# Kernel optimization log

Measured on AMD Instinct MI355X. Metric: run time of the kernel, lower is better.

## Reference

```python
import jax, jax.numpy as jnp
import numpy as np


def setup_inputs() -> dict:
    key = jax.random.key(0)
    k1, k2 = jax.random.split(key)
    B, N1, N2, D = 16, 2048, 2048, 300
    X = jax.random.normal(k1, (B, N1, D), dtype=jnp.float32)
    Y = jax.random.normal(k2, (B, N2, D), dtype=jnp.float32)
    return {"X": X, "Y": Y}


def reference(X, Y):
    # Bidirectional co-attention, unscaled.
    # M1: (b, n1, n2), M2: (b, n2, n1)
    M1 = jnp.einsum("bnd,bmd->bnm", X, Y)
    M2 = jnp.einsum("bmd,bnd->bmn", Y, X)
    N1 = jax.nn.softmax(M1, axis=2)
    N2 = jax.nn.softmax(M2, axis=2)
    O1 = jnp.einsum("bnm,bmd->bnd", N1, Y)  # (b, n1, d)
    O2 = jnp.einsum("bmn,bnd->bmd", N2, X)  # (b, n2, d)
    A1 = O1 * X
    A2 = O2 * Y
    return jnp.concatenate((A1, A2), axis=1)
```

## Files before the change

### kernel.cpp

```cpp
#include <hip/hip_runtime.h>

typedef _Float16 f16;
typedef __attribute__((ext_vector_type(8))) _Float16 f16x8;
typedef __attribute__((ext_vector_type(4))) _Float16 f16x4;
typedef __attribute__((ext_vector_type(4))) float f32x4;

#define BATCH 16
#define NSEQ  2048
#define DDIM  300
#define DPK   328
#define DPV   304
#define NTP   2056
#define XF_ELEMS (BATCH*NSEQ*DPK)
#define XT_ELEMS (BATCH*DPV*NTP)

__device__ __forceinline__ void gl_lds16(const void* g, void* l) {
  __builtin_amdgcn_global_load_lds((const __attribute__((address_space(1))) unsigned int*)g,
                                   (__attribute__((address_space(3))) unsigned int*)l, 16, 0, 0);
}

__global__ __launch_bounds__(256) void prep_kernel(const float* __restrict__ X,
                                                   const float* __restrict__ Y,
                                                   f16* __restrict__ Xf, f16* __restrict__ Yf,
                                                   f16* __restrict__ XT, f16* __restrict__ YT) {
  __shared__ float tile[32][33];
  int bz   = blockIdx.z;
  int tsel = bz >> 4, b = bz & 15;
  const float* src = tsel ? Y : X;
  f16* dF = tsel ? Yf : Xf;
  f16* dT = tsel ? YT : XT;
  int d0 = blockIdx.y * 32;
  int q0 = blockIdx.x * 32;
  int tid = threadIdx.x;
  int c = tid & 31, rr = tid >> 5;

  #pragma unroll
  for (int i = 0; i < 4; ++i) {
    int qr = rr + i * 8;
    int q = q0 + qr, d = d0 + c;
    float v = 0.f;
    if (q < NSEQ && d < DDIM) v = src[(size_t)b * NSEQ * DDIM + (size_t)q * DDIM + d];
    tile[c][qr] = v;
    if (q < NSEQ && d < DPK) dF[(size_t)b * NSEQ * DPK + (size_t)q * DPK + d] = (f16)v;
  }
  __syncthreads();
  #pragma unroll
  for (int i = 0; i < 4; ++i) {
    int dr = rr + i * 8;
    int d = d0 + dr, q = q0 + c;
    if (d < DPV && q < NTP) dT[(size_t)b * DPV * NTP + (size_t)d * NTP + q] = (f16)tile[dr][c];
  }
}

__global__ __launch_bounds__(512, 1) void attn_kernel(const f16* __restrict__ Xf,
                                                      const f16* __restrict__ Yf,
                                                      const f16* __restrict__ XT,
                                                      const f16* __restrict__ YT,
                                                      float* __restrict__ out) {
  __shared__ __align__(16) f16 Ksh[2][64][DPK];
  __shared__ __align__(16) f16 VTsh[DPV][72];
  __shared__ __align__(16) f16 Psh[4][32][72];
  __shared__ float2 Mx[4][2][16];

  int idx = blockIdx.x;
  int swz = (idx & 7) * 64 + (idx >> 3);
  int qt  = swz & 15;
  int b   = (swz >> 4) & 15;
  int dir = swz >> 8;

  const f16* Qsrc = dir ? Yf : Xf;
  const f16* Ksrc = dir ? Xf : Yf;
  const f16* Vts  = dir ? XT : YT;

  const size_t bq = (size_t)b * NSEQ * DPK;
  const size_t bt = (size_t)b * DPV * NTP;

  int tid = threadIdx.x;
  int lane = tid & 63, wid = tid >> 6;
  int qg = wid >> 1, mem = wid & 1;
  int l15 = lane & 15, g = lane >> 4;
  int qbase = qt * 128 + qg * 32;

  f16x8 qf[2][10];
  #pragma unroll
  for (int qi = 0; qi < 2; ++qi) {
    const f16* qrow = Qsrc + bq + (size_t)(qbase + qi * 16 + l15) * DPK + g * 8;
    #pragma unroll
    for (int ks = 0; ks < 10; ++ks) qf[qi][ks] = *(const f16x8*)(qrow + ks * 32);
  }

  const int dtoff = mem ? 10 : 0;
  const int ndt   = mem ? 9 : 10;

  f32x4 O[10][2];
  #pragma unroll
  for (int dt = 0; dt < 10; ++dt) {
    O[dt][0] = (f32x4){0.f, 0.f, 0.f, 0.f};
    O[dt][1] = (f32x4){0.f, 0.f, 0.f, 0.f};
  }
  float m0 = -3.0e38f, m1 = -3.0e38f;
  float l0 = 0.f, l1 = 0.f;

  const char* gK0 = (const char*)(Ksrc + bq);
  const char* gV0 = (const char*)(Vts + bt);

  auto stageK = [&](int tt, int buf) {
    const char* gK = gK0 + (size_t)tt * (64 * DPK * 2);
    char* lK = (char*)&Ksh[buf][0][0];
    #pragma unroll
    for (int i = 0; i < 6; ++i) {
      int c = i * 512 + tid;
      if (c < 2624) gl_lds16(gK + c * 16, lK + c * 16);
    }
  };
  auto stageV = [&](int tt) {
    const char* gV = gV0 + (size_t)tt * 128;
    char* lV = (char*)&VTsh[0][0];
    #pragma unroll
    for (int i = 0; i < 6; ++i) {
      int c = i * 512 + tid;
      if (c < 2736) {
        int row = (int)((unsigned)c / 9u), slot = c - row * 9;
        gl_lds16(gV + (size_t)row * (NTP * 2) + slot * 16, lV + c * 16);
      }
    }
  };

  stageK(0, 0);
  asm volatile("s_waitcnt vmcnt(0)" ::: "memory");
  __builtin_amdgcn_s_barrier();
  __builtin_amdgcn_sched_barrier(0);

  #pragma unroll 1
  for (int t = 0; t < 32; ++t) {
    int kcur = t & 1;

    f32x4 S[2][2];
    S[0][0] = (f32x4){0.f,0.f,0.f,0.f}; S[0][1] = (f32x4){0.f,0.f,0.f,0.f};
    S[1][0] = (f32x4){0.f,0.f,0.f,0.f}; S[1][1] = (f32x4){0.f,0.f,0.f,0.f};
    __builtin_amdgcn_s_setprio(1);
    if (t > 0) {
      #pragma unroll
      for (int ks = 0; ks < 2; ++ks) {
        f16x8 pb0 = *(const f16x8*)&Psh[qg][l15][ks * 32 + g * 8];
        f16x8 pb1 = *(const f16x8*)&Psh[qg][16 + l15][ks * 32 + g * 8];
        #pragma unroll
        for (int dt = 0; dt < 10; ++dt) {
          if (dt < ndt) {
            f16x8 vf = *(const f16x8*)&VTsh[(dtoff + dt) * 16 + l15][ks * 32 + g * 8];
            O[dt][0] = __builtin_amdgcn_mfma_f32_16x16x32_f16(vf, pb0, O[dt][0], 0, 0, 0);
            O[dt][1] = __builtin_amdgcn_mfma_f32_16x16x32_f16(vf, pb1, O[dt][1], 0, 0, 0);
          }
        }
      }
    }
    #pragma unroll
    for (int ks = 0; ks < 10; ++ks) {
      f16x8 a0 = *(const f16x8*)&Ksh[kcur][mem * 32 + l15][ks * 32 + g * 8];
      f16x8 a1 = *(const f16x8*)&Ksh[kcur][mem * 32 + 16 + l15][ks * 32 + g * 8];
      S[0][0] = __builtin_amdgcn_mfma_f32_16x16x32_f16(a0, qf[0][ks], S[0][0], 0, 0, 0);
      S[0][1] = __builtin_amdgcn_mfma_f32_16x16x32_f16(a0, qf[1][ks], S[0][1], 0, 0, 0);
      S[1][0] = __builtin_amdgcn_mfma_f32_16x16x32_f16(a1, qf[0][ks], S[1][0], 0, 0, 0);
      S[1][1] = __builtin_amdgcn_mfma_f32_16x16x32_f16(a1, qf[1][ks], S[1][1], 0, 0, 0);
    }
    __builtin_amdgcn_s_setprio(0);

    if (t < 31) stageK(t + 1, kcur ^ 1);

    float p0 = fmaxf(fmaxf(fmaxf(S[0][0][0], S[0][0][1]), fmaxf(S[0][0][2], S[0][0][3])),
                     fmaxf(fmaxf(S[1][0][0], S[1][0][1]), fmaxf(S[1][0][2], S[1][0][3])));
    float p1 = fmaxf(fmaxf(fmaxf(S[0][1][0], S[0][1][1]), fmaxf(S[0][1][2], S[0][1][3])),
                     fmaxf(fmaxf(S[1][1][0], S[1][1][1]), fmaxf(S[1][1][2], S[1][1][3])));
    p0 = fmaxf(p0, __shfl_xor(p0, 16, 64)); p0 = fmaxf(p0, __shfl_xor(p0, 32, 64));
    p1 = fmaxf(p1, __shfl_xor(p1, 16, 64)); p1 = fmaxf(p1, __shfl_xor(p1, 32, 64));
    if (g == 0) Mx[qg][mem][l15] = float2{p0, p1};

    asm volatile("s_waitcnt lgkmcnt(0)" ::: "memory");
    __builtin_amdgcn_s_barrier();
    __builtin_amdgcn_sched_barrier(0);

    stageV(t);

    float2 pp = Mx[qg][mem ^ 1][l15];
    float tm0 = fmaxf(p0, pp.x), tm1 = fmaxf(p1, pp.y);

    if (__any(tm0 > m0 + 8.0f)) {
      float mn = fmaxf(m0, tm0), al = __expf(m0 - mn);
      l0 *= al;
      #pragma unroll
      for (int dt = 0; dt < 10; ++dt) {
        O[dt][0][0] *= al; O[dt][0][1] *= al; O[dt][0][2] *= al; O[dt][0][3] *= al;
      }
      m0 = mn;
    }
    if (__any(tm1 > m1 + 8.0f)) {
      float mn = fmaxf(m1, tm1), al = __expf(m1 - mn);
      l1 *= al;
      #pragma unroll
      for (int dt = 0; dt < 10; ++dt) {
        O[dt][1][0] *= al; O[dt][1][1] *= al; O[dt][1][2] *= al; O[dt][1][3] *= al;
      }
      m1 = mn;
    }

    #pragma unroll
    for (int kvt = 0; kvt < 2; ++kvt) {
      f16x4 h0, h1;
      #pragma unroll
      for (int r = 0; r < 4; ++r) {
        float e0 = __expf(S[kvt][0][r] - m0);
        float e1 = __expf(S[kvt][1][r] - m1);
        h0[r] = (f16)e0; h1[r] = (f16)e1;
        l0 += e0; l1 += e1;
      }
      *(f16x4*)&Psh[qg][l15][mem * 32 + kvt * 16 + g * 4]      = h0;
      *(f16x4*)&Psh[qg][16 + l15][mem * 32 + kvt * 16 + g * 4] = h1;
    }

    asm volatile("s_waitcnt lgkmcnt(0) vmcnt(0)" ::: "memory");
    __builtin_amdgcn_s_barrier();
    __builtin_amdgcn_sched_barrier(0);
  }

  {
    __builtin_amdgcn_s_setprio(1);
    #pragma unroll
    for (int ks = 0; ks < 2; ++ks) {
      f16x8 pb0 = *(const f16x8*)&Psh[qg][l15][ks * 32 + g * 8];
      f16x8 pb1 = *(const f16x8*)&Psh[qg][16 + l15][ks * 32 + g * 8];
      #pragma unroll
      for (int dt = 0; dt < 10; ++dt) {
        if (dt < ndt) {
          f16x8 vf = *(const f16x8*)&VTsh[(dtoff + dt) * 16 + l15][ks * 32 + g * 8];
          O[dt][0] = __builtin_amdgcn_mfma_f32_16x16x32_f16(vf, pb0, O[dt][0], 0, 0, 0);
          O[dt][1] = __builtin_amdgcn_mfma_f32_16x16x32_f16(vf, pb1, O[dt][1], 0, 0, 0);
        }
      }
    }
    __builtin_amdgcn_s_setprio(0);
  }

  l0 += __shfl_xor(l0, 16, 64); l0 += __shfl_xor(l0, 32, 64);
  l1 += __shfl_xor(l1, 16, 64); l1 += __shfl_xor(l1, 32, 64);
  if (g == 0) Mx[qg][mem][l15] = float2{l0, l1};
  asm volatile("s_waitcnt lgkmcnt(0)" ::: "memory");
  __builtin_amdgcn_s_barrier();
  __builtin_amdgcn_sched_barrier(0);
  float2 pl = Mx[qg][mem ^ 1][l15];
  float r0 = 1.0f / (l0 + pl.x);
  float r1 = 1.0f / (l1 + pl.y);

  #pragma unroll
  for (int qi = 0; qi < 2; ++qi) {
    float rinv = qi ? r1 : r0;
    int q = qbase + qi * 16 + l15;
    const f16* mrow = Qsrc + bq + (size_t)q * DPK;
    size_t orow = (size_t)b * (4096 * 300) + (size_t)(dir * 2048 + q) * 300;
    #pragma unroll
    for (int dt = 0; dt < 10; ++dt) {
      if (dt < ndt) {
        int d = (dtoff + dt) * 16 + g * 4;
        if (d < 300) {
          f16x4 mu = *(const f16x4*)(mrow + d);
          f32x4 o;
          o[0] = O[dt][qi][0] * rinv * (float)mu[0];
          o[1] = O[dt][qi][1] * rinv * (float)mu[1];
          o[2] = O[dt][qi][2] * rinv * (float)mu[2];
          o[3] = O[dt][qi][3] * rinv * (float)mu[3];
          *(f32x4*)&out[orow + d] = o;
        }
      }
    }
  }
}

extern "C" void kernel_launch(void* const* d_in, const int* in_sizes, int n_in,
                              void* d_out, int out_size, void* d_ws, size_t ws_size,
                              hipStream_t stream) {
  const float* X = (const float*)d_in[0];
  const float* Y = (const float*)d_in[1];
  float* out = (float*)d_out;

  size_t need = (size_t)(2 * XF_ELEMS + 2 * XT_ELEMS) * sizeof(f16);
  if (ws_size < need) return;

  f16* XT = (f16*)d_ws;
  f16* YT = XT + XT_ELEMS;
  f16* Xf = YT + XT_ELEMS;
  f16* Yf = Xf + XF_ELEMS;

  prep_kernel<<<dim3(65, 11, 32), 256, 0, stream>>>(X, Y, Xf, Yf, XT, YT);
  attn_kernel<<<dim3(512), 512, 0, stream>>>(Xf, Yf, XT, YT, out);
}
```

Before: 255.8 us.

## Switch attention MFMAs from 16x16x32 to 32x32x16 tiles with interleaved PV

Replaces the 16x16x32 f16 MFMA tiling with 32x32x16 instructions for both QK^T and PV. Each wave now owns a 32x32 score tile in one accumulator and a 5x32-wide output slice, with the two waves overlapping on d range 144-160. The PV MFMAs are split into two halves interleaved with the QK^T halves to mix the dependency chains. Larger tiles cut LDS fragment loads per FLOP and the number of softmax reductions, at the cost of some redundant PV work in the overlap and different register pressure.

```diff
diff --git a/kernel.cpp b/kernel.cpp
--- a/kernel.cpp
+++ b/kernel.cpp
@@ -4,6 +4,7 @@
 typedef __attribute__((ext_vector_type(8))) _Float16 f16x8;
 typedef __attribute__((ext_vector_type(4))) _Float16 f16x4;
 typedef __attribute__((ext_vector_type(4))) float f32x4;
+typedef __attribute__((ext_vector_type(16))) float f32x16;
 
 #define BATCH 16
 #define NSEQ  2048
@@ -60,7 +61,7 @@
   __shared__ __align__(16) f16 Ksh[2][64][DPK];
   __shared__ __align__(16) f16 VTsh[DPV][72];
   __shared__ __align__(16) f16 Psh[4][32][72];
-  __shared__ float2 Mx[4][2][16];
+  __shared__ float MxS[4][2][32];
 
   int idx = blockIdx.x;
   int swz = (idx & 7) * 64 + (idx >> 3);
@@ -78,28 +79,25 @@
   int tid = threadIdx.x;
   int lane = tid & 63, wid = tid >> 6;
   int qg = wid >> 1, mem = wid & 1;
-  int l15 = lane & 15, g = lane >> 4;
+  int l31 = lane & 31, hi = lane >> 5;
   int qbase = qt * 128 + qg * 32;
 
-  f16x8 qf[2][10];
+  f16x8 qf[20];
+  {
+    const f16* qrow = Qsrc + bq + (size_t)(qbase + l31) * DPK + hi * 8;
+    #pragma unroll
+    for (int ks = 0; ks < 20; ++ks) qf[ks] = *(const f16x8*)(qrow + ks * 16);
+  }
+
+  const int dbase = mem ? 144 : 0;
+  const int dlo   = mem ? 160 : 0;
+
+  f32x16 O[5];
   #pragma unroll
-  for (int qi = 0; qi < 2; ++qi) {
-    const f16* qrow = Qsrc + bq + (size_t)(qbase + qi * 16 + l15) * DPK + g * 8;
-    #pragma unroll
-    for (int ks = 0; ks < 10; ++ks) qf[qi][ks] = *(const f16x8*)(qrow + ks * 32);
-  }
-
-  const int dtoff = mem ? 10 : 0;
-  const int ndt   = mem ? 9 : 10;
-
-  f32x4 O[10][2];
-  #pragma unroll
-  for (int dt = 0; dt < 10; ++dt) {
-    O[dt][0] = (f32x4){0.f, 0.f, 0.f, 0.f};
-    O[dt][1] = (f32x4){0.f, 0.f, 0.f, 0.f};
-  }
-  float m0 = -3.0e38f, m1 = -3.0e38f;
-  float l0 = 0.f, l1 = 0.f;
+  for (int dt = 0; dt < 5; ++dt)
+    #pragma unroll
+    for (int e = 0; e < 16; ++e) O[dt][e] = 0.f;
+  float m = -3.0e38f, l = 0.f;
 
   const char* gK0 = (const char*)(Ksrc + bq);
   const char* gV0 = (const char*)(Vts + bt);
@@ -135,45 +133,53 @@
   for (int t = 0; t < 32; ++t) {
     int kcur = t & 1;
 
-    f32x4 S[2][2];
-    S[0][0] = (f32x4){0.f,0.f,0.f,0.f}; S[0][1] = (f32x4){0.f,0.f,0.f,0.f};
-    S[1][0] = (f32x4){0.f,0.f,0.f,0.f}; S[1][1] = (f32x4){0.f,0.f,0.f,0.f};
+    f32x16 S;
+    #pragma unroll
+    for (int e = 0; e < 16; ++e) S[e] = 0.f;
     __builtin_amdgcn_s_setprio(1);
     if (t > 0) {
       #pragma unroll
       for (int ks = 0; ks < 2; ++ks) {
-        f16x8 pb0 = *(const f16x8*)&Psh[qg][l15][ks * 32 + g * 8];
-        f16x8 pb1 = *(const f16x8*)&Psh[qg][16 + l15][ks * 32 + g * 8];
+        f16x8 pf = *(const f16x8*)&Psh[qg][l31][ks * 16 + hi * 8];
         #pragma unroll
-        for (int dt = 0; dt < 10; ++dt) {
-          if (dt < ndt) {
-            f16x8 vf = *(const f16x8*)&VTsh[(dtoff + dt) * 16 + l15][ks * 32 + g * 8];
-            O[dt][0] = __builtin_amdgcn_mfma_f32_16x16x32_f16(vf, pb0, O[dt][0], 0, 0, 0);
-            O[dt][1] = __builtin_amdgcn_mfma_f32_16x16x32_f16(vf, pb1, O[dt][1], 0, 0, 0);
-          }
+        for (int dt = 0; dt < 5; ++dt) {
+          f16x8 vf = *(const f16x8*)&VTsh[dbase + dt * 32 + l31][ks * 16 + hi * 8];
+          O[dt] = __builtin_amdgcn_mfma_f32_32x32x16_f16(vf, pf, O[dt], 0, 0, 0);
         }
       }
     }
     #pragma unroll
     for (int ks = 0; ks < 10; ++ks) {
-      f16x8 a0 = *(const f16x8*)&Ksh[kcur][mem * 32 + l15][ks * 32 + g * 8];
-      f16x8 a1 = *(const f16x8*)&Ksh[kcur][mem * 32 + 16 + l15][ks * 32 + g * 8];
-      S[0][0] = __builtin_amdgcn_mfma_f32_16x16x32_f16(a0, qf[0][ks], S[0][0], 0, 0, 0);
-      S[0][1] = __builtin_amdgcn_mfma_f32_16x16x32_f16(a0, qf[1][ks], S[0][1], 0, 0, 0);
-      S[1][0] = __builtin_amdgcn_mfma_f32_16x16x32_f16(a1, qf[0][ks], S[1][0], 0, 0, 0);
-      S[1][1] = __builtin_amdgcn_mfma_f32_16x16x32_f16(a1, qf[1][ks], S[1][1], 0, 0, 0);
+      f16x8 a = *(const f16x8*)&Ksh[kcur][mem * 32 + l31][ks * 16 + hi * 8];
+      S = __builtin_amdgcn_mfma_f32_32x32x16_f16(a, qf[ks], S, 0, 0, 0);
+    }
+    if (t > 0) {
+      #pragma unroll
+      for (int ks = 2; ks < 4; ++ks) {
+        f16x8 pf = *(const f16x8*)&Psh[qg][l31][ks * 16 + hi * 8];
+        #pragma unroll
+        for (int dt = 0; dt < 5; ++dt) {
+          f16x8 vf = *(const f16x8*)&VTsh[dbase + dt * 32 + l31][ks * 16 + hi * 8];
+          O[dt] = __builtin_amdgcn_mfma_f32_32x32x16_f16(vf, pf, O[dt], 0, 0, 0);
+        }
+      }
+    }
+    #pragma unroll
+    for (int ks = 10; ks < 20; ++ks) {
+      f16x8 a = *(const f16x8*)&Ksh[kcur][mem * 32 + l31][ks * 16 + hi * 8];
+      S = __builtin_amdgcn_mfma_f32_32x32x16_f16(a, qf[ks], S, 0, 0, 0);
     }
     __builtin_amdgcn_s_setprio(0);
 
     if (t < 31) stageK(t + 1, kcur ^ 1);
 
-    float p0 = fmaxf(fmaxf(fmaxf(S[0][0][0], S[0][0][1]), fmaxf(S[0][0][2], S[0][0][3])),
-                     fmaxf(fmaxf(S[1][0][0], S[1][0][1]), fmaxf(S[1][0][2], S[1][0][3])));
-    float p1 = fmaxf(fmaxf(fmaxf(S[0][1][0], S[0][1][1]), fmaxf(S[0][1][2], S[0][1][3])),
-                     fmaxf(fmaxf(S[1][1][0], S[1][1][1]), fmaxf(S[1][1][2], S[1][1][3])));
-    p0 = fmaxf(p0, __shfl_xor(p0, 16, 64)); p0 = fmaxf(p0, __shfl_xor(p0, 32, 64));
-    p1 = fmaxf(p1, __shfl_xor(p1, 16, 64)); p1 = fmaxf(p1, __shfl_xor(p1, 32, 64));
-    if (g == 0) Mx[qg][mem][l15] = float2{p0, p1};
+    float p = fmaxf(fmaxf(fmaxf(S[0], S[1]), S[2]),
+                    fmaxf(fmaxf(S[3], S[4]), S[5]));
+    p = fmaxf(p, fmaxf(fmaxf(S[6], S[7]), fmaxf(S[8], S[9])));
+    p = fmaxf(p, fmaxf(fmaxf(S[10], S[11]), fmaxf(S[12], S[13])));
+    p = fmaxf(p, fmaxf(S[14], S[15]));
+    p = fmaxf(p, __shfl_xor(p, 32, 64));
+    if (lane < 32) MxS[qg][mem][l31] = p;
 
     asm volatile("s_waitcnt lgkmcnt(0)" ::: "memory");
     __builtin_amdgcn_s_barrier();
@@ -181,40 +187,29 @@
 
     stageV(t);
 
-    float2 pp = Mx[qg][mem ^ 1][l15];
-    float tm0 = fmaxf(p0, pp.x), tm1 = fmaxf(p1, pp.y);
-
-    if (__any(tm0 > m0 + 8.0f)) {
-      float mn = fmaxf(m0, tm0), al = __expf(m0 - mn);
-      l0 *= al;
-      #pragma unroll
-      for (int dt = 0; dt < 10; ++dt) {
-        O[dt][0][0] *= al; O[dt][0][1] *= al; O[dt][0][2] *= al; O[dt][0][3] *= al;
-      }
-      m0 = mn;
-    }
-    if (__any(tm1 > m1 + 8.0f)) {
-      float mn = fmaxf(m1, tm1), al = __expf(m1 - mn);
-      l1 *= al;
-      #pragma unroll
-      for (int dt = 0; dt < 10; ++dt) {
-        O[dt][1][0] *= al; O[dt][1][1] *= al; O[dt][1][2] *= al; O[dt][1][3] *= al;
-      }
-      m1 = mn;
-    }
-
-    #pragma unroll
-    for (int kvt = 0; kvt < 2; ++kvt) {
-      f16x4 h0, h1;
-      #pragma unroll
-      for (int r = 0; r < 4; ++r) {
-        float e0 = __expf(S[kvt][0][r] - m0);
-        float e1 = __expf(S[kvt][1][r] - m1);
-        h0[r] = (f16)e0; h1[r] = (f16)e1;
-        l0 += e0; l1 += e1;
-      }
-      *(f16x4*)&Psh[qg][l15][mem * 32 + kvt * 16 + g * 4]      = h0;
-      *(f16x4*)&Psh[qg][16 + l15][mem * 32 + kvt * 16 + g * 4] = h1;
+    float pp = MxS[qg][mem ^ 1][l31];
+    float tm = fmaxf(p, pp);
+
+    if (__any(tm > m + 8.0f)) {
+      float mn = fmaxf(m, tm), al = __expf(m - mn);
+      l *= al;
+      #pragma unroll
+      for (int dt = 0; dt < 5; ++dt)
+        #pragma unroll
+        for (int e = 0; e < 16; ++e) O[dt][e] *= al;
+      m = mn;
+    }
+
+    #pragma unroll
+    for (int r = 0; r < 4; ++r) {
+      f16x4 h;
+      #pragma unroll
+      for (int j = 0; j < 4; ++j) {
+        float e = __expf(S[4 * r + j] - m);
+        h[j] = (f16)e;
+        l += e;
+      }
+      *(f16x4*)&Psh[qg][l31][mem * 32 + r * 8 + hi * 4] = h;
     }
 
     asm volatile("s_waitcnt lgkmcnt(0) vmcnt(0)" ::: "memory");
@@ -225,49 +220,42 @@
   {
     __builtin_amdgcn_s_setprio(1);
     #pragma unroll
-    for (int ks = 0; ks < 2; ++ks) {
-      f16x8 pb0 = *(const f16x8*)&Psh[qg][l15][ks * 32 + g * 8];
-      f16x8 pb1 = *(const f16x8*)&Psh[qg][16 + l15][ks * 32 + g * 8];
-      #pragma unroll
-      for (int dt = 0; dt < 10; ++dt) {
-        if (dt < ndt) {
-          f16x8 vf = *(const f16x8*)&VTsh[(dtoff + dt) * 16 + l15][ks * 32 + g * 8];
-          O[dt][0] = __builtin_amdgcn_mfma_f32_16x16x32_f16(vf, pb0, O[dt][0], 0, 0, 0);
-          O[dt][1] = __builtin_amdgcn_mfma_f32_16x16x32_f16(vf, pb1, O[dt][1], 0, 0, 0);
-        }
+    for (int ks = 0; ks < 4; ++ks) {
+      f16x8 pf = *(const f16x8*)&Psh[qg][l31][ks * 16 + hi * 8];
+      #pragma unroll
+      for (int dt = 0; dt < 5; ++dt) {
+        f16x8 vf = *(const f16x8*)&VTsh[dbase + dt * 32 + l31][ks * 16 + hi * 8];
+        O[dt] = __builtin_amdgcn_mfma_f32_32x32x16_f16(vf, pf, O[dt], 0, 0, 0);
       }
     }
     __builtin_amdgcn_s_setprio(0);
   }
 
-  l0 += __shfl_xor(l0, 16, 64); l0 += __shfl_xor(l0, 32, 64);
-  l1 += __shfl_xor(l1, 16, 64); l1 += __shfl_xor(l1, 32, 64);
-  if (g == 0) Mx[qg][mem][l15] = float2{l0, l1};
+  l += __shfl_xor(l, 32, 64);
+  if (lane < 32) MxS[qg][mem][l31] = l;
   asm volatile("s_waitcnt lgkmcnt(0)" ::: "memory");
   __builtin_amdgcn_s_barrier();
   __builtin_amdgcn_sched_barrier(0);
-  float2 pl = Mx[qg][mem ^ 1][l15];
-  float r0 = 1.0f / (l0 + pl.x);
-  float r1 = 1.0f / (l1 + pl.y);
-
-  #pragma unroll
-  for (int qi = 0; qi < 2; ++qi) {
-    float rinv = qi ? r1 : r0;
-    int q = qbase + qi * 16 + l15;
+  float pl = MxS[qg][mem ^ 1][l31];
+  float rinv = 1.0f / (l + pl);
+
+  {
+    int q = qbase + l31;
     const f16* mrow = Qsrc + bq + (size_t)q * DPK;
     size_t orow = (size_t)b * (4096 * 300) + (size_t)(dir * 2048 + q) * 300;
     #pragma unroll
-    for (int dt = 0; dt < 10; ++dt) {
-      if (dt < ndt) {
-        int d = (dtoff + dt) * 16 + g * 4;
-        if (d < 300) {
-          f16x4 mu = *(const f16x4*)(mrow + d);
+    for (int dt = 0; dt < 5; ++dt) {
+      #pragma unroll
+      for (int r = 0; r < 4; ++r) {
+        int d0 = dbase + dt * 32 + r * 8 + hi * 4;
+        if (d0 >= dlo && d0 < 300) {
+          f16x4 mu = *(const f16x4*)(mrow + d0);
           f32x4 o;
-          o[0] = O[dt][qi][0] * rinv * (float)mu[0];
-          o[1] = O[dt][qi][1] * rinv * (float)mu[1];
-          o[2] = O[dt][qi][2] * rinv * (float)mu[2];
-          o[3] = O[dt][qi][3] * rinv * (float)mu[3];
-          *(f32x4*)&out[orow + d] = o;
+          o[0] = O[dt][4 * r + 0] * rinv * (float)mu[0];
+          o[1] = O[dt][4 * r + 1] * rinv * (float)mu[1];
+          o[2] = O[dt][4 * r + 2] * rinv * (float)mu[2];
+          o[3] = O[dt][4 * r + 3] * rinv * (float)mu[3];
+          *(f32x4*)&out[orow + d0] = o;
         }
       }
     }
```

Result: faster. 244.4 us (-4.5%).
